# Kernel optimization log

Measured on AMD Instinct MI355X. Metric: run time of the kernel, lower is better.

## Reference

```python
import jax, jax.numpy as jnp
import numpy as np

DIM = 1024
NUM_HEADS = 16
HEAD_DIM = DIM // NUM_HEADS
LN_EPS = 1e-5


def setup_inputs() -> dict:
    key = jax.random.key(0)
    ks = jax.random.split(key, 12)
    B, S = 2, 2048
    queries = jax.random.normal(ks[0], (B, S, DIM), dtype=jnp.float32)
    keys = jax.random.normal(ks[1], (B, S, DIM), dtype=jnp.float32)
    values = jax.random.normal(ks[2], (B, S, DIM), dtype=jnp.float32)
    # per-head Linear(dim, head_dim) weights stacked over heads: [H, dim, head_dim]
    scale = 1.0 / np.sqrt(DIM)
    Wq = jax.random.uniform(ks[3], (NUM_HEADS, DIM, HEAD_DIM), jnp.float32, -scale, scale)
    bq = jax.random.uniform(ks[4], (NUM_HEADS, HEAD_DIM), jnp.float32, -scale, scale)
    Wk = jax.random.uniform(ks[5], (NUM_HEADS, DIM, HEAD_DIM), jnp.float32, -scale, scale)
    bk = jax.random.uniform(ks[6], (NUM_HEADS, HEAD_DIM), jnp.float32, -scale, scale)
    Wv = jax.random.uniform(ks[7], (NUM_HEADS, DIM, HEAD_DIM), jnp.float32, -scale, scale)
    bv = jax.random.uniform(ks[8], (NUM_HEADS, HEAD_DIM), jnp.float32, -scale, scale)
    gamma = jnp.ones((DIM,), dtype=jnp.float32)
    beta = jnp.zeros((DIM,), dtype=jnp.float32)
    return {"queries": queries, "keys": keys, "values": values,
            "Wq": Wq, "bq": bq, "Wk": Wk, "bk": bk, "Wv": Wv, "bv": bv,
            "gamma": gamma, "beta": beta}


def reference(queries, keys, values, Wq, bq, Wk, bk, Wv, bv, gamma, beta):
    # Per-head projections fused as a single batched GEMM over heads.
    # q/k/v: [B, H, S, head_dim]  (dropout is identity in eval mode)
    q = jnp.einsum('bsd,hdk->bhsk', queries, Wq) + bq[None, :, None, :]
    k = jnp.einsum('bsd,hdk->bhsk', keys, Wk) + bk[None, :, None, :]
    v = jnp.einsum('bsd,hdk->bhsk', values, Wv) + bv[None, :, None, :]
    # scores: [B, H, S, S], scaled by 1/sqrt(head_dim)
    scores = jnp.einsum('bhsk,bhtk->bhst', q, k) / jnp.sqrt(jnp.float32(HEAD_DIM))
    probs = jax.nn.softmax(scores, axis=-1)
    attended = jnp.einsum('bhst,bhtk->bhsk', probs, v)  # [B, H, S, head_dim]
    # concat heads -> [B, S, dim]
    B, H, S, K = attended.shape
    attended = attended.transpose(0, 2, 1, 3).reshape(B, S, H * K)
    # LayerNorm over last dim
    mean = jnp.mean(attended, axis=-1, keepdims=True)
    var = jnp.mean(jnp.square(attended - mean), axis=-1, keepdims=True)
    normed = (attended - mean) * jax.lax.rsqrt(var + LN_EPS)
    return normed * gamma + beta
```

## Files before the change

kernel.cpp:

```cpp
#include <hip/hip_runtime.h>

#define B_ 2
#define S_ 2048
#define D_ 1024
#define H_ 16
#define HD_ 64

typedef unsigned short u16;
typedef short bf16x8 __attribute__((ext_vector_type(8)));
typedef float f32x4 __attribute__((ext_vector_type(4)));

union FragU { bf16x8 v; u16 u[8]; uint2 d2[2]; unsigned w[4]; uint4 q; };

__device__ __forceinline__ u16 f2bf(float f) {
  unsigned int x = __builtin_bit_cast(unsigned int, f);
  x += 0x7fffu + ((x >> 16) & 1u);
  return (u16)(x >> 16);
}

__device__ __forceinline__ float fexp2(float x) {
  return __builtin_amdgcn_exp2f(x);
}

__device__ __forceinline__ void g2l(const void* g, void* l) {
  __builtin_amdgcn_global_load_lds(
      (const __attribute__((address_space(1))) unsigned int*)g,
      (__attribute__((address_space(3))) unsigned int*)l, 16, 0, 0);
}

#define MFMA16(a, b, c) __builtin_amdgcn_mfma_f32_16x16x32_bf16(a, b, c, 0, 0, 0)

#define KPERM(m) ((((m) & 15) >> 2) * 8 + (((m) >> 4) << 2) + ((m) & 3))

__global__ __launch_bounds__(256) void prep_kernel(
    const float* __restrict__ Wq, const float* __restrict__ Wk,
    const float* __restrict__ Wv, u16* __restrict__ WT)
{
  const int blk = blockIdx.x;
  const int z = blk >> 6, h = (blk >> 2) & 15, qtr = blk & 3;
  const float* src = ((z == 0) ? Wq : (z == 1) ? Wk : Wv) + (size_t)h * D_ * HD_;
  u16* dst = WT + (size_t)z * D_ * D_ + (size_t)h * HD_ * D_;
  const int tid = threadIdx.x;
  const int n = tid & 63, kh = tid >> 6;
  #pragma unroll
  for (int k32 = qtr * 2; k32 < qtr * 2 + 2; ++k32) {
    const int kbase = kh * 256 + k32 * 32;
    union { u16 u[32]; uint4 q[4]; } pk;
    #pragma unroll
    for (int m = 0; m < 32; ++m)
      pk.u[KPERM(m)] = f2bf(src[(size_t)(kbase + m) * HD_ + n]);
    #pragma unroll
    for (int j = 0; j < 4; ++j)
      *(uint4*)(dst + (size_t)n * D_ + kbase + j * 8) = pk.q[j];
  }
}

__global__ __launch_bounds__(512) void proj_kernel(
    const float* __restrict__ Xq, const float* __restrict__ Xk, const float* __restrict__ Xv,
    const u16* __restrict__ WT,
    const float* __restrict__ bq, const float* __restrict__ bk, const float* __restrict__ bv,
    u16* __restrict__ qo, u16* __restrict__ ko, u16* __restrict__ vo)
{
  const int z = blockIdx.z;
  const int rowb = blockIdx.x;
  const int col  = blockIdx.y;
  const float* X  = (z == 0) ? Xq : (z == 1) ? Xk : Xv;
  const float* Bb = (z == 0) ? bq : (z == 1) ? bk : bv;
  u16* out = (z == 0) ? qo : (z == 1) ? ko : vo;
  const float scale = (z == 0) ? 0.125f * 1.44269504f : 1.0f;

  const int tid = threadIdx.x;
  const int l = tid & 63, w = tid >> 6;
  const int g = l >> 4, lr = l & 15;
  const int wm = w >> 1, wn = w & 1;

  __shared__ u16 As_[2][128 * 64];
  __shared__ u16 Bs_[2][128 * 64];

  const char* Wb = (const char*)(WT + (size_t)z * D_ * D_ + (size_t)col * 128 * D_);

  int bOff[2], bLds[2];
  #pragma unroll
  for (int i = 0; i < 2; ++i) {
    const int chunk = tid + i * 512;
    const int br = chunk >> 3, cb = (chunk & 7) * 16;
    bOff[i] = br * 2048 + (cb ^ ((br & 7) << 4));
    bLds[i] = (w * 64 + i * 512) * 16;
  }

  const int arow  = tid >> 2;
  const int aksub = (tid >> 1) & 1;
  const int ag0   = (tid & 1) * 2;
  const float* aSrc = X + (size_t)(rowb * 128 + arow) * D_ + aksub * 32 + ag0 * 4;
  const int asw = (arow & 7) << 4;
  const int aw0 = arow * 128 + ((aksub * 64 + ag0 * 16) ^ asw);
  const int aw1 = arow * 128 + ((aksub * 64 + (ag0 + 1) * 16) ^ asw);

  float4 a0, a1, a2, a3;

#define ALOAD(k0)                                                              \
  {                                                                            \
    const float* s = aSrc + (k0);                                              \
    a0 = *(const float4*)s;        a1 = *(const float4*)(s + 16);              \
    a2 = *(const float4*)(s + 4);  a3 = *(const float4*)(s + 20);              \
  }

#define AWRITE(buf)                                                            \
  {                                                                            \
    FragU t0, t1;                                                              \
    asm("v_cvt_pk_bf16_f32 %0, %1, %2" : "=v"(t0.w[0]) : "v"(a0.x), "v"(a0.y));\
    asm("v_cvt_pk_bf16_f32 %0, %1, %2" : "=v"(t0.w[1]) : "v"(a0.z), "v"(a0.w));\
    asm("v_cvt_pk_bf16_f32 %0, %1, %2" : "=v"(t0.w[2]) : "v"(a1.x), "v"(a1.y));\
    asm("v_cvt_pk_bf16_f32 %0, %1, %2" : "=v"(t0.w[3]) : "v"(a1.z), "v"(a1.w));\
    asm("v_cvt_pk_bf16_f32 %0, %1, %2" : "=v"(t1.w[0]) : "v"(a2.x), "v"(a2.y));\
    asm("v_cvt_pk_bf16_f32 %0, %1, %2" : "=v"(t1.w[1]) : "v"(a2.z), "v"(a2.w));\
    asm("v_cvt_pk_bf16_f32 %0, %1, %2" : "=v"(t1.w[2]) : "v"(a3.x), "v"(a3.y));\
    asm("v_cvt_pk_bf16_f32 %0, %1, %2" : "=v"(t1.w[3]) : "v"(a3.z), "v"(a3.w));\
    *(uint4*)((char*)As_[buf] + aw0) = t0.q;                                   \
    *(uint4*)((char*)As_[buf] + aw1) = t1.q;                                   \
  }

  ALOAD(0);
  AWRITE(0);
  #pragma unroll
  for (int i = 0; i < 2; ++i) g2l(Wb + bOff[i], (char*)Bs_[0] + bLds[i]);
  __syncthreads();

  const f32x4 zero = {0.f, 0.f, 0.f, 0.f};
  f32x4 acc[2][4];
  #pragma unroll
  for (int mt = 0; mt < 2; ++mt)
    #pragma unroll
    for (int nt = 0; nt < 4; ++nt) acc[mt][nt] = zero;

  for (int ks = 0; ks < 16; ++ks) {
    const int cur = ks & 1;
    if (ks < 15) {
      ALOAD((ks + 1) * 64);
      #pragma unroll
      for (int i = 0; i < 2; ++i)
        g2l(Wb + bOff[i] + (ks + 1) * 128, (char*)Bs_[cur ^ 1] + bLds[i]);
    }

    const char* Ac = (const char*)As_[cur];
    const char* Bc = (const char*)Bs_[cur];
    #pragma unroll
    for (int ksub = 0; ksub < 2; ++ksub) {
      FragU aF[2], bF[4];
      #pragma unroll
      for (int mt = 0; mt < 2; ++mt) {
        const int row = wm * 32 + mt * 16 + lr;
        aF[mt].v = *(const bf16x8*)(Ac + row * 128 +
                    ((ksub * 64 + g * 16) ^ ((row & 7) << 4)));
      }
      #pragma unroll
      for (int nt = 0; nt < 4; ++nt) {
        const int row = wn * 64 + nt * 16 + lr;
        bF[nt].v = *(const bf16x8*)(Bc + row * 128 +
                    ((ksub * 64 + g * 16) ^ ((row & 7) << 4)));
      }
      __builtin_amdgcn_s_setprio(1);
      #pragma unroll
      for (int mt = 0; mt < 2; ++mt)
        #pragma unroll
        for (int nt = 0; nt < 4; ++nt)
          acc[mt][nt] = MFMA16(aF[mt].v, bF[nt].v, acc[mt][nt]);
      __builtin_amdgcn_s_setprio(0);
    }

    if (ks < 15) AWRITE(cur ^ 1);
    __syncthreads();
  }

  #pragma unroll
  for (int nt = 0; nt < 4; ++nt) {
    const int ng = col * 128 + wn * 64 + nt * 16 + lr;
    const float bias = Bb[ng];
    const int h = ng >> 6, n = ng & 63;
    const int dperm = (n & 32) + ((n & 15) >> 2) * 8 + ((n & 16) >> 4) * 4 + (n & 3);
    #pragma unroll
    for (int mt = 0; mt < 2; ++mt) {
      const int R = rowb * 128 + wm * 32 + mt * 16 + g * 4;
      const int b = R >> 11, s0 = R & (S_ - 1);
      if (z < 2) {
        #pragma unroll
        for (int r = 0; r < 4; ++r)
          out[(((size_t)b * H_ + h) * S_ + s0 + r) * HD_ + dperm] =
              f2bf((acc[mt][nt][r] + bias) * scale);
      } else {
        const int a = (s0 >> 2) & 7;
        const int s0p = (s0 & ~31) + ((2 * (a & 3) + (a >> 2)) << 2);
        union { u16 u[4]; uint2 d; } pk;
        #pragma unroll
        for (int r = 0; r < 4; ++r) pk.u[r] = f2bf(acc[mt][nt][r] + bias);
        *(uint2*)(out + (((size_t)b * H_ + h) * HD_ + n) * S_ + s0p) = pk.d;
      }
    }
  }
#undef ALOAD
#undef AWRITE
}

__global__ __launch_bounds__(512) void attn_kernel(
    const u16* __restrict__ q, const u16* __restrict__ k,
    const u16* __restrict__ vt, u16* __restrict__ attP, float* __restrict__ lrow)
{
  const int bid = blockIdx.x;
  const int xcd = bid & 7;
  const int t1 = bid >> 3;
  const int qt = t1 & 7;
  const int bh = ((t1 >> 3) << 3) | xcd;

  const int tid = threadIdx.x;
  const int l = tid & 63, w = tid >> 6;
  const int g = l >> 4, lr = l & 15;
  const int qbase = qt * 256 + w * 32;

  #define BUFSZ (64 * 144)
  __shared__ __align__(16) char Ksm[2 * BUFSZ];
  __shared__ __align__(16) char Vsm[2 * BUFSZ];

  FragU qf[2][2];
  #pragma unroll
  for (int qg = 0; qg < 2; ++qg) {
    const char* qrow = (const char*)(q + ((size_t)bh * S_ + qbase + qg * 16 + lr) * HD_);
    qf[qg][0].v = *(const bf16x8*)(qrow + g * 16);
    qf[qg][1].v = *(const bf16x8*)(qrow + 64 + g * 16);
  }

  const char* kByte = (const char*)(k + (size_t)bh * S_ * HD_);
  const char* vByte = (const char*)(vt + (size_t)bh * HD_ * S_);

  const int off = tid * 16;
  const int rr = off >> 7, cc = off & 127;
  char* kD0 = Ksm + rr * 144 + cc;
  char* vD0 = Vsm + rr * 144 + cc;
  const char* kS0 = kByte + off;
  const char* vS0 = vByte + (size_t)rr * (S_ * 2) + cc;

  uint4 kA = *(const uint4*)kS0;
  uint4 vA = *(const uint4*)vS0;
  *(uint4*)kD0 = kA;
  *(uint4*)vD0 = vA;
  __syncthreads();

  const f32x4 zero = {0.f, 0.f, 0.f, 0.f};
  f32x4 accO[2][4] = {{zero, zero, zero, zero}, {zero, zero, zero, zero}};
  float m_[2] = {-3e38f, -3e38f};
  float l_[2] = {0.f, 0.f};

  const char* kfb = Ksm + lr * 144 + g * 16;
  const char* vfb = Vsm + lr * 144 + g * 16;

  for (int t0 = 0; t0 < S_; t0 += 64) {
    const int cur = (t0 >> 6) & 1;
    const bool hasNext = (t0 + 64) < S_;
    if (hasNext) {
      kA = *(const uint4*)(kS0 + (t0 + 64) * 128);
      vA = *(const uint4*)(vS0 + (t0 + 64) * 2);
    }
    const char* kfbc = kfb + cur * BUFSZ;
    const char* vfbc = vfb + cur * BUFSZ;

    f32x4 sc[2][4] = {{zero, zero, zero, zero}, {zero, zero, zero, zero}};
    __builtin_amdgcn_s_setprio(1);
    #pragma unroll
    for (int ct = 0; ct < 4; ++ct) {
      FragU kf0, kf1;
      kf0.v = *(const bf16x8*)(kfbc + ct * 2304);
      kf1.v = *(const bf16x8*)(kfbc + ct * 2304 + 64);
      sc[0][ct] = MFMA16(kf0.v, qf[0][0].v, sc[0][ct]);
      sc[0][ct] = MFMA16(kf1.v, qf[0][1].v, sc[0][ct]);
      sc[1][ct] = MFMA16(kf0.v, qf[1][0].v, sc[1][ct]);
      sc[1][ct] = MFMA16(kf1.v, qf[1][1].v, sc[1][ct]);
    }
    __builtin_amdgcn_s_setprio(0);

    float lmax[2];
    #pragma unroll
    for (int qg = 0; qg < 2; ++qg) {
      float a0 = fmaxf(fmaxf(sc[qg][0][0], sc[qg][0][1]), fmaxf(sc[qg][0][2], sc[qg][0][3]));
      float a1 = fmaxf(fmaxf(sc[qg][1][0], sc[qg][1][1]), fmaxf(sc[qg][1][2], sc[qg][1][3]));
      float a2 = fmaxf(fmaxf(sc[qg][2][0], sc[qg][2][1]), fmaxf(sc[qg][2][2], sc[qg][2][3]));
      float a3 = fmaxf(fmaxf(sc[qg][3][0], sc[qg][3][1]), fmaxf(sc[qg][3][2], sc[qg][3][3]));
      lmax[qg] = fmaxf(fmaxf(a0, a1), fmaxf(a2, a3));
    }
    if (__any((lmax[0] - m_[0] > 8.f) || (lmax[1] - m_[1] > 8.f))) {
      #pragma unroll
      for (int qg = 0; qg < 2; ++qg) {
        float mm = lmax[qg];
        mm = fmaxf(mm, __shfl_xor(mm, 16));
        mm = fmaxf(mm, __shfl_xor(mm, 32));
        const float mn = fmaxf(m_[qg], mm);
        const float al = fexp2(m_[qg] - mn);
        m_[qg] = mn;
        l_[qg] *= al;
        float alr[4];
        #pragma unroll
        for (int r = 0; r < 4; ++r) alr[r] = __shfl(al, g * 4 + r);
        #pragma unroll
        for (int dt = 0; dt < 4; ++dt)
          #pragma unroll
          for (int r = 0; r < 4; ++r) accO[qg][dt][r] *= alr[r];
      }
    }

    FragU pf[2][2];
    #pragma unroll
    for (int qg = 0; qg < 2; ++qg) {
      #pragma unroll
      for (int ct = 0; ct < 4; ++ct)
        #pragma unroll
        for (int r = 0; r < 4; ++r)
          sc[qg][ct][r] = fexp2(sc[qg][ct][r] - m_[qg]);
      float s0 = (sc[qg][0][0] + sc[qg][0][1]) + (sc[qg][0][2] + sc[qg][0][3]);
      float s1 = (sc[qg][1][0] + sc[qg][1][1]) + (sc[qg][1][2] + sc[qg][1][3]);
      float s2 = (sc[qg][2][0] + sc[qg][2][1]) + (sc[qg][2][2] + sc[qg][2][3]);
      float s3 = (sc[qg][3][0] + sc[qg][3][1]) + (sc[qg][3][2] + sc[qg][3][3]);
      l_[qg] += (s0 + s1) + (s2 + s3);
      #pragma unroll
      for (int tc = 0; tc < 2; ++tc) {
        asm("v_cvt_pk_bf16_f32 %0, %1, %2" : "=v"(pf[qg][tc].w[0]) : "v"(sc[qg][2*tc][0]),   "v"(sc[qg][2*tc][1]));
        asm("v_cvt_pk_bf16_f32 %0, %1, %2" : "=v"(pf[qg][tc].w[1]) : "v"(sc[qg][2*tc][2]),   "v"(sc[qg][2*tc][3]));
        asm("v_cvt_pk_bf16_f32 %0, %1, %2" : "=v"(pf[qg][tc].w[2]) : "v"(sc[qg][2*tc+1][0]), "v"(sc[qg][2*tc+1][1]));
        asm("v_cvt_pk_bf16_f32 %0, %1, %2" : "=v"(pf[qg][tc].w[3]) : "v"(sc[qg][2*tc+1][2]), "v"(sc[qg][2*tc+1][3]));
      }
    }

    __builtin_amdgcn_s_setprio(1);
    #pragma unroll
    for (int dt = 0; dt < 4; ++dt) {
      FragU vf0, vf1;
      vf0.v = *(const bf16x8*)(vfbc + dt * 2304);
      vf1.v = *(const bf16x8*)(vfbc + dt * 2304 + 64);
      accO[0][dt] = MFMA16(pf[0][0].v, vf0.v, accO[0][dt]);
      accO[0][dt] = MFMA16(pf[0][1].v, vf1.v, accO[0][dt]);
      accO[1][dt] = MFMA16(pf[1][0].v, vf0.v, accO[1][dt]);
      accO[1][dt] = MFMA16(pf[1][1].v, vf1.v, accO[1][dt]);
    }
    __builtin_amdgcn_s_setprio(0);

    if (hasNext) {
      const int nb = (cur ^ 1) * BUFSZ;
      *(uint4*)(kD0 + nb) = kA;
      *(uint4*)(vD0 + nb) = vA;
    }
    __syncthreads();
  }

  const int b = bh >> 4, h = bh & (H_ - 1);
  u16* basep = attP + (size_t)b * S_ * D_;
  #pragma unroll
  for (int qg = 0; qg < 2; ++qg) {
    float lt = l_[qg];
    lt += __shfl_xor(lt, 16);
    lt += __shfl_xor(lt, 32);
    #pragma unroll
    for (int r = 0; r < 4; ++r) {
      const int s = qbase + qg * 16 + g * 4 + r;
      u16* op = basep + (size_t)s * D_ + h * HD_;
      #pragma unroll
      for (int dt = 0; dt < 4; ++dt) op[dt * 16 + lr] = f2bf(accO[qg][dt][r]);
    }
    if (g == 0)
      lrow[((size_t)b * H_ + h) * S_ + qbase + qg * 16 + lr] = lt;
  }
  #undef BUFSZ
}

__global__ __launch_bounds__(256) void combine_ln_kernel(
    const u16* __restrict__ attP, const float* __restrict__ lrow,
    const float* __restrict__ gamma, const float* __restrict__ beta,
    float* __restrict__ out)
{
  const int row = blockIdx.x;
  const int b = row >> 11, s = row & (S_ - 1);
  const int tid = threadIdx.x;
  const int h = tid >> 4;

  const float inv = 1.0f / lrow[((size_t)b * H_ + h) * S_ + s];
  union { uint2 d; u16 u[4]; } raw;
  raw.d = ((const uint2*)(attP + (size_t)row * D_))[tid];
  float4 x;
  x.x = __builtin_bit_cast(float, (unsigned)raw.u[0] << 16) * inv;
  x.y = __builtin_bit_cast(float, (unsigned)raw.u[1] << 16) * inv;
  x.z = __builtin_bit_cast(float, (unsigned)raw.u[2] << 16) * inv;
  x.w = __builtin_bit_cast(float, (unsigned)raw.u[3] << 16) * inv;

  float sm = x.x + x.y + x.z + x.w;
  float sq = x.x * x.x + x.y * x.y + x.z * x.z + x.w * x.w;
  #pragma unroll
  for (int j = 1; j < 64; j <<= 1) { sm += __shfl_xor(sm, j); sq += __shfl_xor(sq, j); }
  __shared__ float ls[4], lq[4];
  const int w = tid >> 6;
  if ((tid & 63) == 0) { ls[w] = sm; lq[w] = sq; }
  __syncthreads();
  if (tid == 0) {
    ls[0] = ls[0] + ls[1] + ls[2] + ls[3];
    lq[0] = lq[0] + lq[1] + lq[2] + lq[3];
  }
  __syncthreads();
  const float mean = ls[0] * (1.f / D_);
  const float var  = lq[0] * (1.f / D_) - mean * mean;
  const float rs = rsqrtf(var + 1e-5f);
  const float4 gv = ((const float4*)gamma)[tid];
  const float4 bv = ((const float4*)beta)[tid];
  float4 o;
  o.x = (x.x - mean) * rs * gv.x + bv.x;
  o.y = (x.y - mean) * rs * gv.y + bv.y;
  o.z = (x.z - mean) * rs * gv.z + bv.z;
  o.w = (x.w - mean) * rs * gv.w + bv.w;
  ((float4*)(out + (size_t)row * D_))[tid] = o;
}

extern "C" void kernel_launch(void* const* d_in, const int* in_sizes, int n_in,
                              void* d_out, int out_size, void* d_ws, size_t ws_size,
                              hipStream_t stream) {
  const float* queries = (const float*)d_in[0];
  const float* keys    = (const float*)d_in[1];
  const float* values  = (const float*)d_in[2];
  const float* Wq = (const float*)d_in[3];
  const float* bq = (const float*)d_in[4];
  const float* Wk = (const float*)d_in[5];
  const float* bk = (const float*)d_in[6];
  const float* Wv = (const float*)d_in[7];
  const float* bv = (const float*)d_in[8];
  const float* gamma = (const float*)d_in[9];
  const float* beta  = (const float*)d_in[10];
  float* out = (float*)d_out;

  const size_t PER = (size_t)B_ * H_ * S_ * HD_;
  u16* q_ws  = (u16*)d_ws;
  u16* k_ws  = q_ws + PER;
  u16* vt_ws = k_ws + PER;
  u16* WT   = vt_ws + PER;
  u16* attP = vt_ws + PER;
  const size_t NOUT = (size_t)B_ * S_ * D_;
  float* lrow = (float*)(attP + NOUT);

  prep_kernel<<<dim3(192), 256, 0, stream>>>(Wq, Wk, Wv, WT);
  proj_kernel<<<dim3(32, 8, 3), 512, 0, stream>>>(
      queries, keys, values, WT, bq, bk, bv, q_ws, k_ws, vt_ws);
  attn_kernel<<<dim3(256), 512, 0, stream>>>(q_ws, k_ws, vt_ws, attP, lrow);
  combine_ln_kernel<<<dim3(4096), 256, 0, stream>>>(attP, lrow, gamma, beta, out);
}
```

Before: 113.6 us.

## Deepen QKV projection GEMM pipeline with two-stage A register prefetch and fine waitcnt

Restructures the projection GEMM main loop into a manually unrolled ping-pong schedule. The fp32 A tile is now prefetched two k-steps ahead using two register sets, and the B tile is staged straight to LDS. The full __syncthreads is replaced with explicit vmcnt(4)/lgkmcnt(0) waits plus s_barrier, so later global loads stay in flight across the barrier. This aims to hide global load latency in the projection phase, at the cost of more registers and fragile hand-counted wait counts.

Result: no change. 113.6 us (-0.0%).

```diff
diff --git a/kernel.cpp b/kernel.cpp
--- a/kernel.cpp
+++ b/kernel.cpp
@@ -96,35 +96,76 @@
   const int aw0 = arow * 128 + ((aksub * 64 + ag0 * 16) ^ asw);
   const int aw1 = arow * 128 + ((aksub * 64 + (ag0 + 1) * 16) ^ asw);
 
-  float4 a0, a1, a2, a3;
-
-#define ALOAD(k0)                                                              \
+  float4 xA0, xA1, xA2, xA3;
+  float4 xB0, xB1, xB2, xB3;
+
+#define BSTG(buf, k0)                                                          \
+  {                                                                            \
+    g2l(Wb + bOff[0] + (k0) * 2, (char*)Bs_[buf] + bLds[0]);                   \
+    g2l(Wb + bOff[1] + (k0) * 2, (char*)Bs_[buf] + bLds[1]);                   \
+    __builtin_amdgcn_sched_barrier(0);   \
+  }
+
+#define ALOADS(p0, p1, p2, p3, k0)                                             \
   {                                                                            \
     const float* s = aSrc + (k0);                                              \
-    a0 = *(const float4*)s;        a1 = *(const float4*)(s + 16);              \
-    a2 = *(const float4*)(s + 4);  a3 = *(const float4*)(s + 20);              \
-  }
-
-#define AWRITE(buf)                                                            \
+    p0 = *(const float4*)s;        p1 = *(const float4*)(s + 16);              \
+    p2 = *(const float4*)(s + 4);  p3 = *(const float4*)(s + 20);              \
+  }
+
+#define AWR(p0, p1, p2, p3, buf)                                               \
   {                                                                            \
     FragU t0, t1;                                                              \
-    asm("v_cvt_pk_bf16_f32 %0, %1, %2" : "=v"(t0.w[0]) : "v"(a0.x), "v"(a0.y));\
-    asm("v_cvt_pk_bf16_f32 %0, %1, %2" : "=v"(t0.w[1]) : "v"(a0.z), "v"(a0.w));\
-    asm("v_cvt_pk_bf16_f32 %0, %1, %2" : "=v"(t0.w[2]) : "v"(a1.x), "v"(a1.y));\
-    asm("v_cvt_pk_bf16_f32 %0, %1, %2" : "=v"(t0.w[3]) : "v"(a1.z), "v"(a1.w));\
-    asm("v_cvt_pk_bf16_f32 %0, %1, %2" : "=v"(t1.w[0]) : "v"(a2.x), "v"(a2.y));\
-    asm("v_cvt_pk_bf16_f32 %0, %1, %2" : "=v"(t1.w[1]) : "v"(a2.z), "v"(a2.w));\
-    asm("v_cvt_pk_bf16_f32 %0, %1, %2" : "=v"(t1.w[2]) : "v"(a3.x), "v"(a3.y));\
-    asm("v_cvt_pk_bf16_f32 %0, %1, %2" : "=v"(t1.w[3]) : "v"(a3.z), "v"(a3.w));\
+    asm("v_cvt_pk_bf16_f32 %0, %1, %2" : "=v"(t0.w[0]) : "v"(p0.x), "v"(p0.y));\
+    asm("v_cvt_pk_bf16_f32 %0, %1, %2" : "=v"(t0.w[1]) : "v"(p0.z), "v"(p0.w));\
+    asm("v_cvt_pk_bf16_f32 %0, %1, %2" : "=v"(t0.w[2]) : "v"(p1.x), "v"(p1.y));\
+    asm("v_cvt_pk_bf16_f32 %0, %1, %2" : "=v"(t0.w[3]) : "v"(p1.z), "v"(p1.w));\
+    asm("v_cvt_pk_bf16_f32 %0, %1, %2" : "=v"(t1.w[0]) : "v"(p2.x), "v"(p2.y));\
+    asm("v_cvt_pk_bf16_f32 %0, %1, %2" : "=v"(t1.w[1]) : "v"(p2.z), "v"(p2.w));\
+    asm("v_cvt_pk_bf16_f32 %0, %1, %2" : "=v"(t1.w[2]) : "v"(p3.x), "v"(p3.y));\
+    asm("v_cvt_pk_bf16_f32 %0, %1, %2" : "=v"(t1.w[3]) : "v"(p3.z), "v"(p3.w));\
     *(uint4*)((char*)As_[buf] + aw0) = t0.q;                                   \
     *(uint4*)((char*)As_[buf] + aw1) = t1.q;                                   \
   }
 
-  ALOAD(0);
-  AWRITE(0);
-  #pragma unroll
-  for (int i = 0; i < 2; ++i) g2l(Wb + bOff[i], (char*)Bs_[0] + bLds[i]);
-  __syncthreads();
+#define COMPUTE(buf)                                                           \
+  {                                                                            \
+    const char* Ac = (const char*)As_[buf];                                    \
+    const char* Bc = (const char*)Bs_[buf];                                    \
+    _Pragma("unroll")                                                          \
+    for (int ksub = 0; ksub < 2; ++ksub) {                                     \
+      FragU aF[2], bF[4];                                                      \
+      _Pragma("unroll")                                                        \
+      for (int mt = 0; mt < 2; ++mt) {                                         \
+        const int row = wm * 32 + mt * 16 + lr;                                \
+        aF[mt].v = *(const bf16x8*)(Ac + row * 128 +                           \
+                    ((ksub * 64 + g * 16) ^ ((row & 7) << 4)));                \
+      }                                                                        \
+      _Pragma("unroll")                                                        \
+      for (int nt = 0; nt < 4; ++nt) {                                         \
+        const int row = wn * 64 + nt * 16 + lr;                                \
+        bF[nt].v = *(const bf16x8*)(Bc + row * 128 +                           \
+                    ((ksub * 64 + g * 16) ^ ((row & 7) << 4)));                \
+      }                                                                        \
+      __builtin_amdgcn_s_setprio(1);                                           \
+      _Pragma("unroll")                                                        \
+      for (int mt = 0; mt < 2; ++mt)                                           \
+        _Pragma("unroll")                                                      \
+        for (int nt = 0; nt < 4; ++nt)                                         \
+          acc[mt][nt] = MFMA16(aF[mt].v, bF[nt].v, acc[mt][nt]);               \
+      __builtin_amdgcn_s_setprio(0);                                           \
+    }                                                                          \
+  }
+
+#define SYNC4()                                                                \
+  asm volatile("s_waitcnt vmcnt(4) lgkmcnt(0)" ::: "memory");                  \
+  __builtin_amdgcn_s_barrier();                                                \
+  __builtin_amdgcn_sched_barrier(0);
+
+#define SYNC0()                                                                \
+  asm volatile("s_waitcnt vmcnt(0) lgkmcnt(0)" ::: "memory");                  \
+  __builtin_amdgcn_s_barrier();                                                \
+  __builtin_amdgcn_sched_barrier(0);
 
   const f32x4 zero = {0.f, 0.f, 0.f, 0.f};
   f32x4 acc[2][4];
@@ -133,44 +174,31 @@
     #pragma unroll
     for (int nt = 0; nt < 4; ++nt) acc[mt][nt] = zero;
 
-  for (int ks = 0; ks < 16; ++ks) {
-    const int cur = ks & 1;
-    if (ks < 15) {
-      ALOAD((ks + 1) * 64);
-      #pragma unroll
-      for (int i = 0; i < 2; ++i)
-        g2l(Wb + bOff[i] + (ks + 1) * 128, (char*)Bs_[cur ^ 1] + bLds[i]);
-    }
-
-    const char* Ac = (const char*)As_[cur];
-    const char* Bc = (const char*)Bs_[cur];
-    #pragma unroll
-    for (int ksub = 0; ksub < 2; ++ksub) {
-      FragU aF[2], bF[4];
-      #pragma unroll
-      for (int mt = 0; mt < 2; ++mt) {
-        const int row = wm * 32 + mt * 16 + lr;
-        aF[mt].v = *(const bf16x8*)(Ac + row * 128 +
-                    ((ksub * 64 + g * 16) ^ ((row & 7) << 4)));
-      }
-      #pragma unroll
-      for (int nt = 0; nt < 4; ++nt) {
-        const int row = wn * 64 + nt * 16 + lr;
-        bF[nt].v = *(const bf16x8*)(Bc + row * 128 +
-                    ((ksub * 64 + g * 16) ^ ((row & 7) << 4)));
-      }
-      __builtin_amdgcn_s_setprio(1);
-      #pragma unroll
-      for (int mt = 0; mt < 2; ++mt)
-        #pragma unroll
-        for (int nt = 0; nt < 4; ++nt)
-          acc[mt][nt] = MFMA16(aF[mt].v, bF[nt].v, acc[mt][nt]);
-      __builtin_amdgcn_s_setprio(0);
-    }
-
-    if (ks < 15) AWRITE(cur ^ 1);
-    __syncthreads();
-  }
+  ALOADS(xA0, xA1, xA2, xA3, 0);
+  AWR(xA0, xA1, xA2, xA3, 0);
+  BSTG(0, 0);
+  ALOADS(xB0, xB1, xB2, xB3, 64);
+  SYNC4();
+
+  for (int i = 0; i < 7; ++i) {
+    const int e = 2 * i;
+    BSTG(1, (e + 1) * 64);
+    ALOADS(xA0, xA1, xA2, xA3, (e + 2) * 64);
+    COMPUTE(0);
+    AWR(xB0, xB1, xB2, xB3, 1);
+    SYNC4();
+    BSTG(0, (e + 2) * 64);
+    ALOADS(xB0, xB1, xB2, xB3, (e + 3) * 64);
+    COMPUTE(1);
+    AWR(xA0, xA1, xA2, xA3, 0);
+    SYNC4();
+  }
+
+  BSTG(1, 15 * 64);
+  COMPUTE(0);
+  AWR(xB0, xB1, xB2, xB3, 1);
+  SYNC0();
+  COMPUTE(1);
 
   #pragma unroll
   for (int nt = 0; nt < 4; ++nt) {
@@ -197,8 +225,12 @@
       }
     }
   }
-#undef ALOAD
-#undef AWRITE
+#undef BSTG
+#undef ALOADS
+#undef AWR
+#undef COMPUTE
+#undef SYNC4
+#undef SYNC0
 }
 
 __global__ __launch_bounds__(512) void attn_kernel(
```
